# Performance work log

Measured on AMD Instinct MI355X. Metric: run time of the kernel, lower is better.

The kernel has to match this reference:

```python
import jax, jax.numpy as jnp
import numpy as np

EMBED_DIM = 768
NUM_HEADS = 12
HEAD_DIM = EMBED_DIM // NUM_HEADS
SCALE = HEAD_DIM ** -0.5


def setup_inputs() -> dict:
    key = jax.random.key(0)
    ks = jax.random.split(key, 9)
    B, S, D = 2, 2048, EMBED_DIM
    init = 1.0 / np.sqrt(D)  # ~ nn.Linear default uniform scale
    x = jax.random.normal(ks[0], (B, S, D), dtype=jnp.float32)
    Wq = jax.random.uniform(ks[1], (D, D), jnp.float32, -init, init)
    bq = jax.random.uniform(ks[2], (D,), jnp.float32, -init, init)
    Wk = jax.random.uniform(ks[3], (D, D), jnp.float32, -init, init)
    bk = jax.random.uniform(ks[4], (D,), jnp.float32, -init, init)
    Wv = jax.random.uniform(ks[5], (D, D), jnp.float32, -init, init)
    bv = jax.random.uniform(ks[6], (D,), jnp.float32, -init, init)
    Wo = jax.random.uniform(ks[7], (D, D), jnp.float32, -init, init)
    bo = jax.random.uniform(ks[8], (D,), jnp.float32, -init, init)
    return {"x": x, "Wq": Wq, "bq": bq, "Wk": Wk, "bk": bk,
            "Wv": Wv, "bv": bv, "Wo": Wo, "bo": bo}


def reference(x, Wq, bq, Wk, bk, Wv, bv, Wo, bo):
    B, S, D = x.shape
    H, Dh = NUM_HEADS, HEAD_DIM
    # projections; weights stored as (in, out) so x @ W == torch Linear with W.T
    q = (x @ Wq + bq).reshape(B, S, H, Dh).transpose(0, 2, 1, 3)  # [B,H,S,Dh]
    k = (x @ Wk + bk).reshape(B, S, H, Dh).transpose(0, 2, 1, 3)
    v = (x @ Wv + bv).reshape(B, S, H, Dh).transpose(0, 2, 1, 3)
    scores = jnp.einsum("bhqd,bhkd->bhqk", q, k) * SCALE        # [B,H,S,S]
    weights = jax.nn.softmax(scores, axis=-1)
    out = jnp.einsum("bhqk,bhkd->bhqd", weights, v)              # [B,H,S,Dh]
    out = out.transpose(0, 2, 1, 3).reshape(B, S, D)
    return out @ Wo + bo
```

## Files before the change

### kernel.cpp

```cpp
#include <hip/hip_runtime.h>
#include <math.h>

#define BB 2
#define SS 2048
#define DDIM 768
#define HH 12
#define DH 64
#define NROWS (BB*SS)
#define NTOK_D (NROWS*DDIM)

typedef _Float16 f16;
typedef _Float16 half4 __attribute__((ext_vector_type(4)));
typedef _Float16 half8 __attribute__((ext_vector_type(8)));
typedef float f32x4 __attribute__((ext_vector_type(4)));

#define MFMA16(a,b,c) __builtin_amdgcn_mfma_f32_16x16x32_f16((a),(b),(c),0,0,0)
#define QSCALE (0.125f * 1.44269504088896f)

__device__ __forceinline__ int swz(int row, int chunk16) {
    return row*128 + ((chunk16 ^ (row & 7)) << 4);
}

__global__ __launch_bounds__(256) void prep_x(const float* __restrict__ x, f16* __restrict__ xh)
{
    int i = blockIdx.x * 256 + threadIdx.x;
    const float4* in = (const float4*)x;
    float4 a = in[i*2], b = in[i*2+1];
    half8 h = {(f16)a.x,(f16)a.y,(f16)a.z,(f16)a.w,(f16)b.x,(f16)b.y,(f16)b.z,(f16)b.w};
    *(half8*)(xh + (size_t)i*8) = h;
}

__global__ __launch_bounds__(256) void prep_w(const float* __restrict__ Wq, const float* __restrict__ Wk,
                                              const float* __restrict__ Wv, const float* __restrict__ Wo,
                                              f16* __restrict__ Wt)
{
    const int z = blockIdx.z;
    const float* W = z==0 ? Wq : (z==1 ? Wk : (z==2 ? Wv : Wo));
    f16* out = Wt + (size_t)z * DDIM * DDIM;

    __shared__ float tile[64][65];
    const int t = threadIdx.x;
    const int k0 = blockIdx.x*64, n0 = blockIdx.y*64;

    const int kr = t >> 2, nc = (t & 3) * 16;
    #pragma unroll
    for (int i = 0; i < 4; ++i) {
        float4 v = *(const float4*)&W[(size_t)(k0+kr)*DDIM + n0 + nc + i*4];
        tile[kr][nc+i*4+0] = v.x; tile[kr][nc+i*4+1] = v.y;
        tile[kr][nc+i*4+2] = v.z; tile[kr][nc+i*4+3] = v.w;
    }
    __syncthreads();
    const int nr = t >> 2, kc = (t & 3) * 16;
    half8 h0, h1;
    #pragma unroll
    for (int j = 0; j < 8; ++j) {
        h0[j] = (f16)tile[kc + j][nr];
        h1[j] = (f16)tile[kc + 8 + j][nr];
    }
    *(half8*)&out[(size_t)(n0+nr)*DDIM + k0 + kc]     = h0;
    *(half8*)&out[(size_t)(n0+nr)*DDIM + k0 + kc + 8] = h1;
}

__global__ __launch_bounds__(256) void proj_qkv(const f16* __restrict__ Xh, const f16* __restrict__ Wt,
        const float* __restrict__ bq, const float* __restrict__ bk, const float* __restrict__ bv,
        f16* __restrict__ qb, f16* __restrict__ kb2, f16* __restrict__ vtb)
{
    const int z = blockIdx.z;
    const f16* Wz = Wt + (size_t)z * DDIM * DDIM;
    const float* bias = z==0 ? bq : (z==1 ? bk : bv);
    const float qscale = (z==0) ? QSCALE : 1.0f;

    __shared__ __align__(16) unsigned char lds[24*1024];
    unsigned char* As = lds;
    unsigned char* Bs = lds + 8*1024;

    const int tid = threadIdx.x;
    const int l = tid & 63, w = tid >> 6;
    const int wm = w >> 1, wn = w & 1;
    const int m0 = blockIdx.x * 64, n0 = blockIdx.y * 128;

    f32x4 acc[2][4];
    #pragma unroll
    for (int i=0;i<2;i++)
        #pragma unroll
        for (int j=0;j<4;j++) { f32x4 zv = {0.f,0.f,0.f,0.f}; acc[i][j] = zv; }

    for (int k0 = 0; k0 < DDIM; k0 += 64) {
        __syncthreads();
        #pragma unroll
        for (int i = 0; i < 2; ++i) {
            int c = tid + i*256;
            int row = c >> 3, kc = c & 7;
            half8 v = *(const half8*)&Xh[(size_t)(m0+row)*DDIM + k0 + kc*8];
            *(half8*)(As + swz(row, kc)) = v;
        }
        #pragma unroll
        for (int i = 0; i < 4; ++i) {
            int c = tid + i*256;
            int row = c >> 3, kc = c & 7;
            half8 v = *(const half8*)&Wz[(size_t)(n0+row)*DDIM + k0 + kc*8];
            *(half8*)(Bs + swz(row, kc)) = v;
        }
        __syncthreads();

        half8 af[2][2], bf[4][2];
        #pragma unroll
        for (int mt = 0; mt < 2; ++mt) {
            int row = wm*32 + mt*16 + (l & 15);
            #pragma unroll
            for (int kh = 0; kh < 2; ++kh)
                af[mt][kh] = *(const half8*)(As + swz(row, kh*4 + (l>>4)));
        }
        #pragma unroll
        for (int nt = 0; nt < 4; ++nt) {
            int row = wn*64 + nt*16 + (l & 15);
            #pragma unroll
            for (int kh = 0; kh < 2; ++kh)
                bf[nt][kh] = *(const half8*)(Bs + swz(row, kh*4 + (l>>4)));
        }
        #pragma unroll
        for (int mt = 0; mt < 2; ++mt)
            #pragma unroll
            for (int nt = 0; nt < 4; ++nt) {
                acc[mt][nt] = MFMA16(af[mt][0], bf[nt][0], acc[mt][nt]);
                acc[mt][nt] = MFMA16(af[mt][1], bf[nt][1], acc[mt][nt]);
            }
    }

    if (z == 2) {
        #pragma unroll
        for (int mt = 0; mt < 2; ++mt)
            #pragma unroll
            for (int nt = 0; nt < 4; ++nt) {
                int m = m0 + wm*32 + mt*16 + (l>>4)*4;
                int n = n0 + wn*64 + nt*16 + (l & 15);
                int b = m >> 11, s = m & 2047;
                int h = n >> 6,  d = n & 63;
                float bs = bias[n];
                half4 o4 = {(f16)(acc[mt][nt][0] + bs), (f16)(acc[mt][nt][1] + bs),
                            (f16)(acc[mt][nt][2] + bs), (f16)(acc[mt][nt][3] + bs)};
                *(half4*)&vtb[(((size_t)(b*HH + h))*DH + d)*SS + s] = o4;
            }
    } else {
        f16* out = (z == 0) ? qb : kb2;
        #pragma unroll
        for (int mt = 0; mt < 2; ++mt)
            #pragma unroll
            for (int nt = 0; nt < 4; ++nt)
                #pragma unroll
                for (int r = 0; r < 4; ++r) {
                    int m = m0 + wm*32 + mt*16 + (l>>4)*4 + r;
                    int n = n0 + wn*64 + nt*16 + (l & 15);
                    float v = (acc[mt][nt][r] + bias[n]) * qscale;
                    int b = m >> 11, s = m & 2047;
                    int h = n >> 6,  d = n & 63;
                    out[(((size_t)(b*HH + h))*SS + s)*DH + d] = (f16)v;
                }
    }
}

__global__ __launch_bounds__(128) void attn_mfma(
        const f16* __restrict__ qbuf, const f16* __restrict__ kbuf,
        const f16* __restrict__ vtbuf, f16* __restrict__ obuf)
{
    __shared__ __align__(16) unsigned char lds[40*1024];

    const int tid = threadIdx.x;
    const int l = tid & 63, w = tid >> 6;
    const int g = l >> 4, qi = l & 15;
    const int q0 = blockIdx.x * 64 + w * 32;
    const size_t base = ((size_t)(blockIdx.z * HH + blockIdx.y)) * SS * DH;
    unsigned char* Pw = lds + 32*1024 + w*4096;

    half8 qf[2][2];
    #pragma unroll
    for (int f = 0; f < 2; ++f)
        #pragma unroll
        for (int kh = 0; kh < 2; ++kh)
            qf[f][kh] = *(const half8*)&qbuf[base + (size_t)(q0 + f*16 + qi)*DH + kh*32 + g*8];

    f32x4 oacc[2][4];
    #pragma unroll
    for (int f = 0; f < 2; ++f)
        #pragma unroll
        for (int i = 0; i < 4; ++i) { f32x4 zv = {0.f,0.f,0.f,0.f}; oacc[f][i] = zv; }
    float mrun[2] = {-INFINITY, -INFINITY};
    float lsum[2] = {0.f, 0.f};

    half8 sk[4], svv[4];

#define LOADT(t) { \
        _Pragma("unroll") \
        for (int i = 0; i < 4; ++i) { \
            int c = i*128 + tid, row = c >> 3, col = c & 7; \
            sk[i]  = *(const half8*)&kbuf[base + (size_t)((t)*64 + row)*DH + col*8]; \
            svv[i] = *(const half8*)&vtbuf[base + (size_t)row*SS + (t)*64 + col*8]; \
        } }

#define WRT(bufi) { \
        unsigned char* Kb_ = lds + (bufi)*16384; \
        unsigned char* Vb_ = Kb_ + 8192; \
        _Pragma("unroll") \
        for (int i = 0; i < 4; ++i) { \
            int c = i*128 + tid, row = c >> 3, col = c & 7; \
            *(half8*)(Kb_ + swz(row, col)) = sk[i]; \
            *(half8*)(Vb_ + swz(row, col)) = svv[i]; \
        } }

    LOADT(0); WRT(0);
    __syncthreads();

    for (int t = 0; t < 32; ++t) {
        const int cur = t & 1;
        if (t < 31) LOADT(t+1);

        unsigned char* Kb = lds + cur*16384;
        unsigned char* Vb = Kb + 8192;

        half8 kf[8];
        #pragma unroll
        for (int mt = 0; mt < 4; ++mt)
            #pragma unroll
            for (int kh = 0; kh < 2; ++kh)
                kf[mt*2+kh] = *(const half8*)(Kb + swz(mt*16 + qi, kh*4 + g));

        #pragma unroll
        for (int f = 0; f < 2; ++f) {
            f32x4 sv[4];
            #pragma unroll
            for (int mt = 0; mt < 4; ++mt) {
                f32x4 zz = {0.f,0.f,0.f,0.f};
                zz = MFMA16(kf[mt*2+0], qf[f][0], zz);
                sv[mt] = MFMA16(kf[mt*2+1], qf[f][1], zz);
            }
            float lm = -INFINITY;
            #pragma unroll
            for (int mt = 0; mt < 4; ++mt)
                #pragma unroll
                for (int r = 0; r < 4; ++r) lm = fmaxf(lm, sv[mt][r]);
            lm = fmaxf(lm, __shfl_xor(lm, 16));
            lm = fmaxf(lm, __shfl_xor(lm, 32));
            float mnew = fmaxf(mrun[f], lm);
            float fsc = exp2f(mrun[f] - mnew);
            mrun[f] = mnew;
            float rs = 0.f;
            #pragma unroll
            for (int mt = 0; mt < 4; ++mt)
                #pragma unroll
                for (int r = 0; r < 4; ++r) {
                    float pv = exp2f(sv[mt][r] - mnew);
                    sv[mt][r] = pv; rs += pv;
                }
            rs += __shfl_xor(rs, 16);
            rs += __shfl_xor(rs, 32);
            lsum[f] = lsum[f]*fsc + rs;
            #pragma unroll
            for (int dt = 0; dt < 4; ++dt)
                #pragma unroll
                for (int r = 0; r < 4; ++r) oacc[f][dt][r] *= fsc;
            #pragma unroll
            for (int mt = 0; mt < 4; ++mt) {
                half4 pk = {(f16)sv[mt][0], (f16)sv[mt][1], (f16)sv[mt][2], (f16)sv[mt][3]};
                *(half4*)(Pw + swz(f*16 + qi, 2*mt + (g>>1)) + (g&1)*8) = pk;
            }
        }

        half8 vf[8];
        #pragma unroll
        for (int dt = 0; dt < 4; ++dt)
            #pragma unroll
            for (int kh = 0; kh < 2; ++kh)
                vf[dt*2+kh] = *(const half8*)(Vb + swz(dt*16 + qi, kh*4 + g));

        #pragma unroll
        for (int f = 0; f < 2; ++f) {
            half8 pf0 = *(const half8*)(Pw + swz(f*16 + qi, g));
            half8 pf1 = *(const half8*)(Pw + swz(f*16 + qi, 4 + g));
            #pragma unroll
            for (int dt = 0; dt < 4; ++dt) {
                oacc[f][dt] = MFMA16(vf[dt*2+0], pf0, oacc[f][dt]);
                oacc[f][dt] = MFMA16(vf[dt*2+1], pf1, oacc[f][dt]);
            }
        }

        if (t < 31) WRT(cur^1);
        __syncthreads();
    }

    #pragma unroll
    for (int f = 0; f < 2; ++f) {
        const float inv = 1.0f / lsum[f];
        #pragma unroll
        for (int dt = 0; dt < 4; ++dt) {
            half4 o4 = {(f16)(oacc[f][dt][0]*inv), (f16)(oacc[f][dt][1]*inv),
                        (f16)(oacc[f][dt][2]*inv), (f16)(oacc[f][dt][3]*inv)};
            *(half4*)&obuf[base + (size_t)(q0 + f*16 + qi)*DH + dt*16 + g*4] = o4;
        }
    }
#undef LOADT
#undef WRT
}

__global__ __launch_bounds__(256) void proj_out(const f16* __restrict__ obuf, const f16* __restrict__ Wt,
                                                const float* __restrict__ bo, float* __restrict__ out)
{
    const f16* Wz = Wt + (size_t)3 * DDIM * DDIM;

    __shared__ __align__(16) unsigned char lds[24*1024];
    unsigned char* As = lds;
    unsigned char* Bs = lds + 8*1024;

    const int tid = threadIdx.x;
    const int l = tid & 63, w = tid >> 6;
    const int wm = w >> 1, wn = w & 1;
    const int m0 = blockIdx.x * 64, n0 = blockIdx.y * 128;

    f32x4 acc[2][4];
    #pragma unroll
    for (int i=0;i<2;i++)
        #pragma unroll
        for (int j=0;j<4;j++) { f32x4 zv = {0.f,0.f,0.f,0.f}; acc[i][j] = zv; }

    for (int k0 = 0; k0 < DDIM; k0 += 64) {
        const int h = k0 >> 6;
        __syncthreads();
        #pragma unroll
        for (int i = 0; i < 2; ++i) {
            int c = tid + i*256;
            int row = c >> 3, kc = c & 7;
            int m = m0 + row, b = m >> 11, s = m & 2047;
            half8 v = *(const half8*)&obuf[(((size_t)(b*HH + h))*SS + s)*DH + kc*8];
            *(half8*)(As + swz(row, kc)) = v;
        }
        #pragma unroll
        for (int i = 0; i < 4; ++i) {
            int c = tid + i*256;
            int row = c >> 3, kc = c & 7;
            half8 v = *(const half8*)&Wz[(size_t)(n0+row)*DDIM + k0 + kc*8];
            *(half8*)(Bs + swz(row, kc)) = v;
        }
        __syncthreads();

        half8 af[2][2], bf[4][2];
        #pragma unroll
        for (int mt = 0; mt < 2; ++mt) {
            int row = wm*32 + mt*16 + (l & 15);
            #pragma unroll
            for (int kh = 0; kh < 2; ++kh)
                af[mt][kh] = *(const half8*)(As + swz(row, kh*4 + (l>>4)));
        }
        #pragma unroll
        for (int nt = 0; nt < 4; ++nt) {
            int row = wn*64 + nt*16 + (l & 15);
            #pragma unroll
            for (int kh = 0; kh < 2; ++kh)
                bf[nt][kh] = *(const half8*)(Bs + swz(row, kh*4 + (l>>4)));
        }
        #pragma unroll
        for (int mt = 0; mt < 2; ++mt)
            #pragma unroll
            for (int nt = 0; nt < 4; ++nt) {
                acc[mt][nt] = MFMA16(af[mt][0], bf[nt][0], acc[mt][nt]);
                acc[mt][nt] = MFMA16(af[mt][1], bf[nt][1], acc[mt][nt]);
            }
    }

    #pragma unroll
    for (int mt = 0; mt < 2; ++mt)
        #pragma unroll
        for (int nt = 0; nt < 4; ++nt)
            #pragma unroll
            for (int r = 0; r < 4; ++r) {
                int m = m0 + wm*32 + mt*16 + (l>>4)*4 + r;
                int n = n0 + wn*64 + nt*16 + (l & 15);
                out[(size_t)m*DDIM + n] = acc[mt][nt][r] + bo[n];
            }
}

extern "C" void kernel_launch(void* const* d_in, const int* in_sizes, int n_in,
                              void* d_out, int out_size, void* d_ws, size_t ws_size,
                              hipStream_t stream)
{
    const float* x  = (const float*)d_in[0];
    const float* Wq = (const float*)d_in[1];
    const float* bq = (const float*)d_in[2];
    const float* Wk = (const float*)d_in[3];
    const float* bk = (const float*)d_in[4];
    const float* Wv = (const float*)d_in[5];
    const float* bv = (const float*)d_in[6];
    const float* Wo = (const float*)d_in[7];
    const float* bo = (const float*)d_in[8];

    char* ws = (char*)d_ws;
    const size_t XH_B  = (size_t)NTOK_D * 2;
    const size_t WT_B  = (size_t)4 * DDIM * DDIM * 2;
    const size_t HB_B  = (size_t)BB * HH * SS * DH * 2;

    f16* Xh = (f16*)ws;
    f16* Wt = (f16*)(ws + XH_B);
    f16* qb = (f16*)(ws + XH_B + WT_B);
    f16* kb = (f16*)(ws + XH_B + WT_B + HB_B);
    f16* vt = (f16*)(ws + XH_B + WT_B + 2*HB_B);
    f16* ob = (f16*)(ws + XH_B + WT_B + 3*HB_B);

    prep_x<<<NTOK_D/(256*8), 256, 0, stream>>>(x, Xh);
    prep_w<<<dim3(DDIM/64, DDIM/64, 4), 256, 0, stream>>>(Wq, Wk, Wv, Wo, Wt);
    proj_qkv<<<dim3(NROWS/64, DDIM/128, 3), 256, 0, stream>>>(Xh, Wt, bq, bk, bv, qb, kb, vt);
    attn_mfma<<<dim3(SS/64, HH, BB), 128, 0, stream>>>(qb, kb, vt, ob);
    proj_out<<<dim3(NROWS/64, DDIM/128), 256, 0, stream>>>(ob, Wt, bo, (float*)d_out);
}
```

Measured before the change: 134.0 us.

## Split attention keys in halves with combine kernel, lazy rescale, single-buffered LDS

Attention now splits the key range into two halves across blockIdx.z, doubling the grid to use more CUs. Each half writes a normalized partial output plus its running max and sum, and a new combine kernel merges the two halves. The online softmax skips the rescale of the accumulator unless the row max grows by more than a threshold, and MFMA sections get raised wave priority. LDS is reduced to a single K/V buffer with two barriers per tile to raise occupancy, at the cost of losing the double-buffer overlap and adding an extra launch plus partial-result traffic.

```diff
diff --git a/kernel.cpp b/kernel.cpp
--- a/kernel.cpp
+++ b/kernel.cpp
@@ -8,6 +8,7 @@
 #define DH 64
 #define NROWS (BB*SS)
 #define NTOK_D (NROWS*DDIM)
+#define NQT (SS/64)
 
 typedef _Float16 f16;
 typedef _Float16 half4 __attribute__((ext_vector_type(4)));
@@ -16,6 +17,7 @@
 
 #define MFMA16(a,b,c) __builtin_amdgcn_mfma_f32_16x16x32_f16((a),(b),(c),0,0,0)
 #define QSCALE (0.125f * 1.44269504088896f)
+#define DEFER_THR 8.0f
 
 __device__ __forceinline__ int swz(int row, int chunk16) {
     return row*128 + ((chunk16 ^ (row & 7)) << 4);
@@ -161,16 +163,23 @@
 
 __global__ __launch_bounds__(128) void attn_mfma(
         const f16* __restrict__ qbuf, const f16* __restrict__ kbuf,
-        const f16* __restrict__ vtbuf, f16* __restrict__ obuf)
-{
-    __shared__ __align__(16) unsigned char lds[40*1024];
+        const f16* __restrict__ vtbuf, f16* __restrict__ pO, float2* __restrict__ mlb)
+{
+    __shared__ __align__(16) unsigned char lds[24*1024];
 
     const int tid = threadIdx.x;
     const int l = tid & 63, w = tid >> 6;
     const int g = l >> 4, qi = l & 15;
-    const int q0 = blockIdx.x * 64 + w * 32;
-    const size_t base = ((size_t)(blockIdx.z * HH + blockIdx.y)) * SS * DH;
-    unsigned char* Pw = lds + 32*1024 + w*4096;
+    const int qt = blockIdx.x, h = blockIdx.y;
+    const int b = blockIdx.z >> 1, khalf = blockIdx.z & 1;
+    const int q0 = qt * 64 + w * 32;
+    const size_t base = ((size_t)(b * HH + h)) * SS * DH;
+    const int key0 = khalf * (SS/2);
+    const int pid = (b * HH + h) * NQT + qt;
+
+    unsigned char* Kb = lds;
+    unsigned char* Vb = lds + 8192;
+    unsigned char* Pw = lds + 16384 + w*4096;
 
     half8 qf[2][2];
     #pragma unroll
@@ -193,29 +202,23 @@
         _Pragma("unroll") \
         for (int i = 0; i < 4; ++i) { \
             int c = i*128 + tid, row = c >> 3, col = c & 7; \
-            sk[i]  = *(const half8*)&kbuf[base + (size_t)((t)*64 + row)*DH + col*8]; \
-            svv[i] = *(const half8*)&vtbuf[base + (size_t)row*SS + (t)*64 + col*8]; \
+            sk[i]  = *(const half8*)&kbuf[base + (size_t)(key0 + (t)*64 + row)*DH + col*8]; \
+            svv[i] = *(const half8*)&vtbuf[base + (size_t)row*SS + key0 + (t)*64 + col*8]; \
         } }
 
-#define WRT(bufi) { \
-        unsigned char* Kb_ = lds + (bufi)*16384; \
-        unsigned char* Vb_ = Kb_ + 8192; \
+#define WRT { \
         _Pragma("unroll") \
         for (int i = 0; i < 4; ++i) { \
             int c = i*128 + tid, row = c >> 3, col = c & 7; \
-            *(half8*)(Kb_ + swz(row, col)) = sk[i]; \
-            *(half8*)(Vb_ + swz(row, col)) = svv[i]; \
+            *(half8*)(Kb + swz(row, col)) = sk[i]; \
+            *(half8*)(Vb + swz(row, col)) = svv[i]; \
         } }
 
-    LOADT(0); WRT(0);
+    LOADT(0); WRT;
     __syncthreads();
 
-    for (int t = 0; t < 32; ++t) {
-        const int cur = t & 1;
-        if (t < 31) LOADT(t+1);
-
-        unsigned char* Kb = lds + cur*16384;
-        unsigned char* Vb = Kb + 8192;
+    for (int t = 0; t < 16; ++t) {
+        if (t < 15) LOADT(t+1);
 
         half8 kf[8];
         #pragma unroll
@@ -223,16 +226,24 @@
             #pragma unroll
             for (int kh = 0; kh < 2; ++kh)
                 kf[mt*2+kh] = *(const half8*)(Kb + swz(mt*16 + qi, kh*4 + g));
+        half8 vf[8];
+        #pragma unroll
+        for (int dt = 0; dt < 4; ++dt)
+            #pragma unroll
+            for (int kh = 0; kh < 2; ++kh)
+                vf[dt*2+kh] = *(const half8*)(Vb + swz(dt*16 + qi, kh*4 + g));
 
         #pragma unroll
         for (int f = 0; f < 2; ++f) {
             f32x4 sv[4];
+            __builtin_amdgcn_s_setprio(1);
             #pragma unroll
             for (int mt = 0; mt < 4; ++mt) {
                 f32x4 zz = {0.f,0.f,0.f,0.f};
                 zz = MFMA16(kf[mt*2+0], qf[f][0], zz);
                 sv[mt] = MFMA16(kf[mt*2+1], qf[f][1], zz);
             }
+            __builtin_amdgcn_s_setprio(0);
             float lm = -INFINITY;
             #pragma unroll
             for (int mt = 0; mt < 4; ++mt)
@@ -240,24 +251,27 @@
                 for (int r = 0; r < 4; ++r) lm = fmaxf(lm, sv[mt][r]);
             lm = fmaxf(lm, __shfl_xor(lm, 16));
             lm = fmaxf(lm, __shfl_xor(lm, 32));
-            float mnew = fmaxf(mrun[f], lm);
-            float fsc = exp2f(mrun[f] - mnew);
-            mrun[f] = mnew;
+            if (!__all(lm <= mrun[f] + DEFER_THR)) {
+                float mnew = fmaxf(mrun[f], lm);
+                float fsc = exp2f(mrun[f] - mnew);
+                mrun[f] = mnew;
+                lsum[f] *= fsc;
+                #pragma unroll
+                for (int dt = 0; dt < 4; ++dt)
+                    #pragma unroll
+                    for (int r = 0; r < 4; ++r) oacc[f][dt][r] *= fsc;
+            }
             float rs = 0.f;
             #pragma unroll
             for (int mt = 0; mt < 4; ++mt)
                 #pragma unroll
                 for (int r = 0; r < 4; ++r) {
-                    float pv = exp2f(sv[mt][r] - mnew);
+                    float pv = exp2f(sv[mt][r] - mrun[f]);
                     sv[mt][r] = pv; rs += pv;
                 }
             rs += __shfl_xor(rs, 16);
             rs += __shfl_xor(rs, 32);
-            lsum[f] = lsum[f]*fsc + rs;
-            #pragma unroll
-            for (int dt = 0; dt < 4; ++dt)
-                #pragma unroll
-                for (int r = 0; r < 4; ++r) oacc[f][dt][r] *= fsc;
+            lsum[f] += rs;
             #pragma unroll
             for (int mt = 0; mt < 4; ++mt) {
                 half4 pk = {(f16)sv[mt][0], (f16)sv[mt][1], (f16)sv[mt][2], (f16)sv[mt][3]};
@@ -265,40 +279,74 @@
             }
         }
 
-        half8 vf[8];
-        #pragma unroll
-        for (int dt = 0; dt < 4; ++dt)
-            #pragma unroll
-            for (int kh = 0; kh < 2; ++kh)
-                vf[dt*2+kh] = *(const half8*)(Vb + swz(dt*16 + qi, kh*4 + g));
-
         #pragma unroll
         for (int f = 0; f < 2; ++f) {
             half8 pf0 = *(const half8*)(Pw + swz(f*16 + qi, g));
             half8 pf1 = *(const half8*)(Pw + swz(f*16 + qi, 4 + g));
+            __builtin_amdgcn_s_setprio(1);
             #pragma unroll
             for (int dt = 0; dt < 4; ++dt) {
                 oacc[f][dt] = MFMA16(vf[dt*2+0], pf0, oacc[f][dt]);
                 oacc[f][dt] = MFMA16(vf[dt*2+1], pf1, oacc[f][dt]);
             }
-        }
-
-        if (t < 31) WRT(cur^1);
-        __syncthreads();
-    }
-
+            __builtin_amdgcn_s_setprio(0);
+        }
+
+        if (t < 15) {
+            __syncthreads();
+            WRT;
+            __syncthreads();
+        }
+    }
+
+    f16* po = pO + ((size_t)pid*2 + khalf) * (64*64);
+    float2* mlp = mlb + ((size_t)pid*2 + khalf) * 64;
     #pragma unroll
     for (int f = 0; f < 2; ++f) {
+        const int qw = w*32 + f*16 + qi;
         const float inv = 1.0f / lsum[f];
         #pragma unroll
         for (int dt = 0; dt < 4; ++dt) {
             half4 o4 = {(f16)(oacc[f][dt][0]*inv), (f16)(oacc[f][dt][1]*inv),
                         (f16)(oacc[f][dt][2]*inv), (f16)(oacc[f][dt][3]*inv)};
-            *(half4*)&obuf[base + (size_t)(q0 + f*16 + qi)*DH + dt*16 + g*4] = o4;
-        }
+            *(half4*)&po[qw*64 + dt*16 + g*4] = o4;
+        }
+        if (g == 0) mlp[qw] = make_float2(mrun[f], lsum[f]);
     }
 #undef LOADT
 #undef WRT
+}
+
+__global__ __launch_bounds__(256) void attn_combine(
+        const f16* __restrict__ pO, const float2* __restrict__ mlb, f16* __restrict__ ob)
+{
+    const int pid = blockIdx.x;
+    const int q = threadIdx.x >> 2, dg = (threadIdx.x & 3) << 4;
+    const f16* O0 = pO + (size_t)pid*2*(64*64);
+    const f16* O1 = O0 + 64*64;
+    float2 a = mlb[(pid*2+0)*64 + q];
+    float2 c = mlb[(pid*2+1)*64 + q];
+    float M = fmaxf(a.x, c.x);
+    float w0 = exp2f(a.x - M) * a.y;
+    float w1 = exp2f(c.x - M) * c.y;
+    float inv = 1.0f / (w0 + w1);
+    w0 *= inv; w1 *= inv;
+
+    half8 x0 = *(const half8*)&O0[q*64 + dg];
+    half8 x1 = *(const half8*)&O0[q*64 + dg + 8];
+    half8 y0 = *(const half8*)&O1[q*64 + dg];
+    half8 y1 = *(const half8*)&O1[q*64 + dg + 8];
+    half8 r0, r1;
+    #pragma unroll
+    for (int j = 0; j < 8; ++j) {
+        r0[j] = (f16)(w0*(float)x0[j] + w1*(float)y0[j]);
+        r1[j] = (f16)(w0*(float)x1[j] + w1*(float)y1[j]);
+    }
+    const int bh = pid >> 5, qt = pid & 31;
+    const int s = qt*64 + q;
+    f16* dst = &ob[((size_t)bh*SS + s)*DH + dg];
+    *(half8*)dst = r0;
+    *(half8*)(dst + 8) = r1;
 }
 
 __global__ __launch_bounds__(256) void proj_out(const f16* __restrict__ obuf, const f16* __restrict__ Wt,
@@ -395,6 +443,7 @@
     const size_t XH_B  = (size_t)NTOK_D * 2;
     const size_t WT_B  = (size_t)4 * DDIM * DDIM * 2;
     const size_t HB_B  = (size_t)BB * HH * SS * DH * 2;
+    const size_t PO_B  = (size_t)BB * HH * NQT * 2 * 64 * 64 * 2;
 
     f16* Xh = (f16*)ws;
     f16* Wt = (f16*)(ws + XH_B);
@@ -402,10 +451,13 @@
     f16* kb = (f16*)(ws + XH_B + WT_B + HB_B);
     f16* vt = (f16*)(ws + XH_B + WT_B + 2*HB_B);
     f16* ob = (f16*)(ws + XH_B + WT_B + 3*HB_B);
+    f16* pO = (f16*)(ws + XH_B + WT_B + 4*HB_B);
+    float2* mlb = (float2*)(ws + XH_B + WT_B + 4*HB_B + PO_B);
 
     prep_x<<<NTOK_D/(256*8), 256, 0, stream>>>(x, Xh);
     prep_w<<<dim3(DDIM/64, DDIM/64, 4), 256, 0, stream>>>(Wq, Wk, Wv, Wo, Wt);
     proj_qkv<<<dim3(NROWS/64, DDIM/128, 3), 256, 0, stream>>>(Xh, Wt, bq, bk, bv, qb, kb, vt);
-    attn_mfma<<<dim3(SS/64, HH, BB), 128, 0, stream>>>(qb, kb, vt, ob);
+    attn_mfma<<<dim3(NQT, HH, BB*2), 128, 0, stream>>>(qb, kb, vt, pO, mlb);
+    attn_combine<<<dim3(BB*HH*NQT), 256, 0, stream>>>(pO, mlb, ob);
     proj_out<<<dim3(NROWS/64, DDIM/128), 256, 0, stream>>>(ob, Wt, bo, (float*)d_out);
 }
```

Measured after the change: 137.9 us. 2.9% more time.
